# Optimization experiments

Measured on AMD Instinct MI355X. Metric: run time of the kernel, lower is better.

The kernel has to match this reference:

```python
import jax, jax.numpy as jnp
import numpy as np

KERNEL_MUL = 2.0
KERNEL_NUM = 5
THRESH = 0.5            # cfg.FIXED_CONFIDENCE_THRESHOLD
LAMBDA = 1.0            # cfg.ECDA_CLASS_ATTENTION_LAMBDA
GAMMA = 0.1             # cfg.ECDA_COMPACTNESS_WEIGHT_GAMMA
DELTA = 0.01            # cfg.ECDA_REPULSION_WEIGHT_DELTA
NUM_CLASSES = 8
N, D = 2048, 256


def _sqdist(a, b):
    # pairwise squared euclidean distances [Na, Nb]
    d2 = (jnp.sum(a * a, 1)[:, None] + jnp.sum(b * b, 1)[None, :]
          - 2.0 * (a @ b.T))
    return jnp.maximum(d2, 0.0)


def setup_inputs() -> dict:
    key = jax.random.key(0)
    ks = jax.random.split(key, 6)
    return {
        'clean_feats': jax.random.normal(ks[0], (N, D), dtype=jnp.float32),
        'noisy_feats': jax.random.normal(ks[1], (N, D), dtype=jnp.float32),
        'clean_labels': jax.random.randint(ks[2], (N,), 0, NUM_CLASSES),
        'noisy_labels': jax.random.randint(ks[3], (N,), 0, NUM_CLASSES),
        'noisy_mask': jax.random.uniform(ks[4], (N,), dtype=jnp.float32),
        'noisy_scores': jax.random.uniform(ks[5], (N,), dtype=jnp.float32),
        'class_weights_wce': jax.random.uniform(jax.random.fold_in(key, 7), (NUM_CLASSES,), dtype=jnp.float32),
    }


def reference(clean_feats, noisy_feats, clean_labels, noisy_labels,
              noisy_mask, noisy_scores, class_weights_wce):
    C = class_weights_wce.shape[0]
    mask_n = noisy_mask > THRESH                       # float mask -> bool (cfg threshold)

    # full pairwise squared-distance matrices, reused by every class
    D_cc = _sqdist(clean_feats, clean_feats)           # [Nc, Nc]
    D_nn = _sqdist(noisy_feats, noisy_feats)           # [Nn, Nn]
    D_cn = _sqdist(clean_feats, noisy_feats)           # [Nc, Nn]

    classes = jnp.arange(C)
    Ms = (clean_labels[None, :] == classes[:, None]).astype(jnp.float32)   # [C, Nc]
    Mn = ((noisy_labels[None, :] == classes[:, None]) & mask_n[None, :]).astype(jnp.float32)  # [C, Nn]

    # noisy centroids + repulsion over valid classes (torch.pdist mean, negated)
    counts_n = Mn.sum(1)
    centroids = (Mn @ noisy_feats) / jnp.maximum(counts_n, 1.0)[:, None]
    valid = counts_n > 0
    Dcen = jnp.sqrt(jnp.maximum(_sqdist(centroids, centroids), 1e-12))
    pair = jnp.triu(jnp.ones((C, C), bool), 1) & valid[:, None] & valid[None, :]
    npairs = pair.sum().astype(jnp.float32)
    repulsion = jnp.where(valid.sum() > 1,
                          -jnp.sum(jnp.where(pair, Dcen, 0.0)) / jnp.maximum(npairs, 1.0),
                          0.0)

    attn = jnp.exp(LAMBDA * (class_weights_wce.mean() - class_weights_wce))
    half = KERNEL_MUL ** (KERNEL_NUM // 2)

    total = jnp.float32(0.0)
    for c in range(C):
        ms = Ms[c]                                     # clean weights (ones, masked)
        mn = Mn[c]
        n_s, n_t = ms.sum(), mn.sum()
        n = n_s + n_t
        # bandwidth from subset L2 sum (detached, as in .data)
        sumL2 = ms @ (D_cc @ ms) + mn @ (D_nn @ mn) + 2.0 * (ms @ (D_cn @ mn))
        sumL2 = jax.lax.stop_gradient(sumL2)
        bw0 = sumL2 / jnp.maximum(n * n - n, 1.0) / half
        wn = noisy_scores * mn                          # masked noisy weights
        ss = tt = st = jnp.float32(0.0)
        for k in range(KERNEL_NUM):
            bw = bw0 * (KERNEL_MUL ** k) + 1e-8
            ss = ss + ms @ (jnp.exp(-D_cc / bw) @ ms)
            tt = tt + wn @ (jnp.exp(-D_nn / bw) @ wn)
            st = st + ms @ (jnp.exp(-D_cn / bw) @ wn)
        sw = wn.sum()
        term_ss = ss / (n_s * n_s + 1e-8)
        term_tt = tt / (sw * sw + 1e-8)
        term_st = st / (n_s * sw + 1e-8)
        mmd = term_ss + term_tt - 2.0 * term_st
        compact = jnp.sum(mn * jnp.sum((noisy_feats - centroids[c]) ** 2, 1)) / jnp.maximum(n_t, 1.0)
        loss_c = mmd + GAMMA * compact + DELTA * repulsion
        total = total + jnp.where((n_s >= 2) & (n_t >= 2), attn[c] * loss_c, 0.0)
    return total
```

## Files before the change

kernel.cpp:

```cpp
#include <hip/hip_runtime.h>
#include <math.h>


static constexpr int NC = 8;
static constexpr int NN = 2048;
static constexpr int DD = 256;

static constexpr int OFF_CNT_S = 0;
static constexpr int OFF_CNT_T = 64;
static constexpr int OFF_SW    = 128;
static constexpr int OFF_COEF  = 192;
static constexpr int OFF_CCOMP = 256;
static constexpr int OFF_SQSP  = 1024;
static constexpr int OFF_SQTP  = 1536;
static constexpr int OFF_HDR   = 2048;
static constexpr int OFF_VSP   = 4096;
static constexpr int OFF_VTP   = 135168;
static constexpr int OFF_VS    = 266240;
static constexpr int OFF_VT    = 274432;
static constexpr int OFF_QBFS  = 282624;
static constexpr int OFF_QBFT  = 348160;
static constexpr int OFF_WTP   = 413696;
static constexpr size_t OFF_PKS = 479232;
static constexpr size_t OFF_PKT = 8867840;

typedef __attribute__((ext_vector_type(8))) short bf16x8;
typedef __attribute__((ext_vector_type(4))) float f32x4;

__device__ inline float wred64(float v) {
  for (int o = 32; o > 0; o >>= 1) v += __shfl_xor(v, o, 64);
  return v;
}
__device__ inline float brs256(float v, float* sh4) {
  for (int o = 32; o > 0; o >>= 1) v += __shfl_xor(v, o, 64);
  int w = threadIdx.x >> 6, ln = threadIdx.x & 63;
  __syncthreads();
  if (ln == 0) sh4[w] = v;
  __syncthreads();
  float r = 0.f;
  if (threadIdx.x == 0) r = sh4[0] + sh4[1] + sh4[2] + sh4[3];
  return r;
}

__global__ __launch_bounds__(256) void ecda_pack(
    const float* __restrict__ cfeat, const float* __restrict__ nfeat,
    const int* __restrict__ clab, const int* __restrict__ nlab,
    const float* __restrict__ nmask, const float* __restrict__ nscore,
    char* __restrict__ ws, float* __restrict__ out) {
  __shared__ int   ls_idx[NN];
  __shared__ float ls_wt[NN];
  __shared__ int   ls_cntw[4];
  __shared__ float ls_mom[4][256];
  __shared__ float ls_sq[4];
  __shared__ float sh4[4];
  int tid = threadIdx.x, bx = blockIdx.x;
  int wv = tid >> 6, lane = tid & 63;
  int typ = bx >> 7, c = (bx >> 4) & 7, chunk = bx & 15;

  if (bx == 0 && tid == 0) out[0] = 0.f;

  const int* labs = typ ? nlab : clab;
  const float* feats = typ ? nfeat : cfeat;

  int rb = wv * 512;
  int lv[8]; float mv[8], sv[8];
#pragma unroll
  for (int it = 0; it < 8; ++it) {
    int i = rb + it * 64 + lane;
    lv[it] = labs[i];
    if (typ) { mv[it] = nmask[i]; sv[it] = nscore[i]; }
  }
  unsigned long long msks[8];
  int cntw = 0;
#pragma unroll
  for (int it = 0; it < 8; ++it) {
    bool m = (lv[it] == c) && (!typ || mv[it] > 0.5f);
    msks[it] = __ballot(m);
    cntw += __popcll(msks[it]);
  }
  if (lane == 0) ls_cntw[wv] = cntw;
  __syncthreads();
  int base = 0;
  for (int w2 = 0; w2 < wv; ++w2) base += ls_cntw[w2];
#pragma unroll
  for (int it = 0; it < 8; ++it) {
    bool m = (msks[it] >> lane) & 1ull;
    int pos = __popcll(msks[it] & ((1ull << lane) - 1ull));
    if (m) {
      ls_idx[base + pos] = rb + it * 64 + lane;
      ls_wt[base + pos] = typ ? sv[it] : 1.f;
    }
    base += __popcll(msks[it]);
  }
  __syncthreads();
  int count = ls_cntw[0] + ls_cntw[1] + ls_cntw[2] + ls_cntw[3];

  if (chunk == 0) {
    if (tid == 0) (typ ? (int*)(ws + OFF_CNT_T) : (int*)(ws + OFF_CNT_S))[c] = count;
    if (typ) {
      float s = 0.f;
      for (int i = tid; i < count; i += 256) s += ls_wt[i];
      s = brs256(s, sh4);
      if (tid == 0) ((float*)(ws + OFF_SW))[c] = s;
    }
  }

  unsigned short* pk = (unsigned short*)(ws + (typ ? OFF_PKT : OFF_PKS)) + (size_t)c * NN * DD;
  float* qarr = (float*)(ws + (typ ? OFF_QBFT : OFF_QBFS)) + c * NN;
  float* wtp  = (float*)(ws + OFF_WTP) + c * NN;
  float vax = 0.f, vay = 0.f, vaz = 0.f, vaw = 0.f, sqa = 0.f;
  int mstart = chunk * 4 + wv;
  for (int m0 = mstart; m0 < count; m0 += 256) {
    int mm[4]; bool act[4]; float4 v[4];
#pragma unroll
    for (int b = 0; b < 4; ++b) {
      int m = m0 + b * 64;
      act[b] = (m < count);
      mm[b] = act[b] ? m : m0;
    }
#pragma unroll
    for (int b = 0; b < 4; ++b) {
      int idx = ls_idx[mm[b]];
      v[b] = *(const float4*)&feats[(size_t)idx * DD + lane * 4];
    }
#pragma unroll
    for (int b = 0; b < 4; ++b) {
      float raw = wred64(v[b].x * v[b].x + v[b].y * v[b].y
                       + v[b].z * v[b].z + v[b].w * v[b].w);
      unsigned ux = __float_as_uint(v[b].x); ux = (ux + 0x7fffu + ((ux >> 16) & 1u)) & 0xffff0000u;
      unsigned uy = __float_as_uint(v[b].y); uy = (uy + 0x7fffu + ((uy >> 16) & 1u)) & 0xffff0000u;
      unsigned uz = __float_as_uint(v[b].z); uz = (uz + 0x7fffu + ((uz >> 16) & 1u)) & 0xffff0000u;
      unsigned uw = __float_as_uint(v[b].w); uw = (uw + 0x7fffu + ((uw >> 16) & 1u)) & 0xffff0000u;
      float rx = __uint_as_float(ux), ry = __uint_as_float(uy);
      float rz = __uint_as_float(uz), rw = __uint_as_float(uw);
      float rq = wred64(rx * rx + ry * ry + rz * rz + rw * rw);
      if (act[b]) {
        vax += v[b].x; vay += v[b].y; vaz += v[b].z; vaw += v[b].w;
        sqa += raw;
        ushort4 b4;
        b4.x = (unsigned short)(ux >> 16); b4.y = (unsigned short)(uy >> 16);
        b4.z = (unsigned short)(uz >> 16); b4.w = (unsigned short)(uw >> 16);
        *(ushort4*)&pk[(size_t)mm[b] * DD + lane * 4] = b4;
        if (lane == 0) {
          qarr[mm[b]] = rq;
          if (typ) wtp[mm[b]] = ls_wt[mm[b]];
        }
      }
    }
  }
  ls_mom[wv][lane * 4 + 0] = vax; ls_mom[wv][lane * 4 + 1] = vay;
  ls_mom[wv][lane * 4 + 2] = vaz; ls_mom[wv][lane * 4 + 3] = vaw;
  if (lane == 0) ls_sq[wv] = sqa;
  __syncthreads();
  float s = ls_mom[0][tid] + ls_mom[1][tid] + ls_mom[2][tid] + ls_mom[3][tid];
  float* vp = (float*)(ws + (typ ? OFF_VTP : OFF_VSP)) + (c * 16 + chunk) * 256;
  vp[tid] = s;
  if (tid == 0)
    ((float*)(ws + (typ ? OFF_SQTP : OFF_SQSP)))[c * 16 + chunk] =
        ls_sq[0] + ls_sq[1] + ls_sq[2] + ls_sq[3];
}

__global__ __launch_bounds__(256) void ecda_scalars(
    const float* __restrict__ cw, char* __restrict__ ws) {
  __shared__ float sh4[4];
  int c = blockIdx.x, tid = threadIdx.x;
  const float* vsp = (const float*)(ws + OFF_VSP);
  const float* vtp = (const float*)(ws + OFF_VTP);
  float vsd = 0.f, vtd = 0.f;
#pragma unroll
  for (int ch = 0; ch < 16; ++ch) {
    vsd += vsp[(c * 16 + ch) * 256 + tid];
    vtd += vtp[(c * 16 + ch) * 256 + tid];
  }
  ((float*)(ws + OFF_VS))[c * 256 + tid] = vsd;
  ((float*)(ws + OFF_VT))[c * 256 + tid] = vtd;
  float dss = brs256(vsd * vsd, sh4);
  float dtt = brs256(vtd * vtd, sh4);
  float dst = brs256(vsd * vtd, sh4);
  if (tid == 0) {
    const float* sqsp = (const float*)(ws + OFF_SQSP);
    const float* sqtp = (const float*)(ws + OFF_SQTP);
    float sqs = 0.f, sqt = 0.f;
    for (int ch = 0; ch < 16; ++ch) { sqs += sqsp[c * 16 + ch]; sqt += sqtp[c * 16 + ch]; }
    int nsi = ((const int*)(ws + OFF_CNT_S))[c];
    int nti = ((const int*)(ws + OFF_CNT_T))[c];
    float ns = (float)nsi, nt = (float)nti, n = ns + nt;
    float sumL2 = 2.f * ns * sqs - 2.f * dss
                + 2.f * nt * sqt - 2.f * dtt
                + 2.f * (nt * sqs + ns * sqt - 2.f * dst);
    float bw0 = sumL2 / fmaxf(n * n - n, 1.f) * 0.25f;
    float ib[5];
    float mul = 1.f;
    for (int k = 0; k < 5; ++k) { ib[k] = 1.f / (bw0 * mul + 1e-8f); mul *= 2.f; }
    float meanw = 0.f;
    for (int c2 = 0; c2 < NC; ++c2) meanw += cw[c2];
    meanw *= (1.f / NC);
    float attn = expf(meanw - cw[c]);
    float coef = (nsi >= 2 && nti >= 2) ? attn : 0.f;
    float swc = ((const float*)(ws + OFF_SW))[c];
    float scc = coef / (ns * ns + 1e-8f);
    float snn = coef / (swc * swc + 1e-8f);
    float scn = -2.f * coef / (ns * swc + 1e-8f);
    float* hdr = (float*)(ws + OFF_HDR);
    for (int ty = 0; ty < 3; ++ty) {
      float* h = hdr + (ty * 8 + c) * 8;
      int na = (ty == 1) ? nti : nsi;
      int nb = (ty == 0) ? nsi : nti;
      h[0] = __int_as_float(na);
      h[1] = __int_as_float(nb);
      h[2] = (ty == 0) ? scc : (ty == 1) ? snn : scn;
      h[3] = ib[0]; h[4] = ib[1]; h[5] = ib[2]; h[6] = ib[3]; h[7] = ib[4];
    }
    float mx = fmaxf(nt, 1.f);
    float compact = (sqt - 2.f * dtt / mx + nt * dtt / (mx * mx)) / mx;
    ((float*)(ws + OFF_COEF))[c] = coef;
    ((float*)(ws + OFF_CCOMP))[c] = coef * 0.1f * compact;
  }
}

__global__ __launch_bounds__(256) void ecda_pairs(
    char* __restrict__ ws, float* __restrict__ out) {
  __shared__ float shred[4];
  __shared__ float dcen[28];
  int tid = threadIdx.x, bx = blockIdx.x;
  int wv = tid >> 6, lane = tid & 63;

  if (bx == 1536) {
    const int* cnt_t = (const int*)(ws + OFF_CNT_T);
    const float* vt = (const float*)(ws + OFF_VT);
    for (int t = wv; t < 28; t += 4) {
      int a = 0, r = t;
      while (r >= 7 - a) { r -= 7 - a; ++a; }
      int b = a + 1 + r;
      float ima = 1.f / fmaxf((float)cnt_t[a], 1.f);
      float imb = 1.f / fmaxf((float)cnt_t[b], 1.f);
      float4 x = *(const float4*)&vt[a * DD + lane * 4];
      float4 y = *(const float4*)&vt[b * DD + lane * 4];
      float dx = x.x * ima - y.x * imb, dy = x.y * ima - y.y * imb;
      float dz = x.z * ima - y.z * imb, dw = x.w * ima - y.w * imb;
      float s = wred64(dx * dx + dy * dy + dz * dz + dw * dw);
      if (lane == 0) dcen[t] = sqrtf(fmaxf(s, 1e-12f));
    }
    __syncthreads();
    if (tid == 0) {
      int nvalid = 0;
      for (int c = 0; c < NC; ++c) nvalid += (cnt_t[c] > 0);
      float sumD = 0.f; int np = 0; int p = 0;
      for (int a = 0; a < NC; ++a)
        for (int b = a + 1; b < NC; ++b) {
          if (cnt_t[a] > 0 && cnt_t[b] > 0) { sumD += dcen[p]; ++np; }
          ++p;
        }
      float repl = (nvalid > 1) ? (-sumD / fmaxf((float)np, 1.f)) : 0.f;
      const float* coefA = (const float*)(ws + OFF_COEF);
      const float* ccomp = (const float*)(ws + OFF_CCOMP);
      float base = 0.f, csum = 0.f;
      for (int c = 0; c < NC; ++c) { base += ccomp[c]; csum += coefA[c]; }
      base += 0.01f * repl * csum;
      atomicAdd(out, base);
    }
    return;
  }

  int type  = bx >> 9;
  int c     = (bx >> 6) & 7;
  int rtile = (bx >> 3) & 7;
  int ctile = bx & 7;
  if (type <= 1 && ctile < rtile) return;

  const f32x4* H = (const f32x4*)((const char*)ws + OFF_HDR) + (type * 8 + c) * 2;
  f32x4 h0 = H[0];
  int na = __float_as_int(h0[0]);
  int nb = __float_as_int(h0[1]);
  float scale = h0[2];
  int rbase = rtile * 32, cbase = ctile * 32;
  if (scale == 0.f || rbase >= na || cbase >= nb) return;
  f32x4 h1 = H[1];
  float ib0 = h0[3], ib1 = h1[0], ib2 = h1[1], ib3 = h1[2], ib4 = h1[3];
  float factor = (type <= 1 && ctile > rtile) ? 2.f : 1.f;

  const unsigned short* pkS = (const unsigned short*)(ws + OFF_PKS) + (size_t)c * NN * DD;
  const unsigned short* pkT = (const unsigned short*)(ws + OFF_PKT) + (size_t)c * NN * DD;
  const float* qbS = (const float*)(ws + OFF_QBFS) + c * NN;
  const float* qbT = (const float*)(ws + OFF_QBFT) + c * NN;
  const float* wtp = (const float*)(ws + OFF_WTP) + c * NN;
  const unsigned short* pkA = (type == 1) ? pkT : pkS;
  const unsigned short* pkB = (type == 0) ? pkS : pkT;
  const float* qaB = (type == 1) ? qbT : qbS;
  const float* qbB = (type == 0) ? qbS : qbT;

  int sr = (wv >> 1) * 16, sc2 = (wv & 1) * 16;
  int posA = rbase + sr + (lane & 15);
  int posB = cbase + sc2 + (lane & 15);
  int pAc = posA < na ? posA : (na - 1);
  int pBc = posB < nb ? posB : (nb - 1);
  const unsigned short* rowA = pkA + (size_t)pAc * DD + (lane >> 4) * 8;
  const unsigned short* rowB = pkB + (size_t)pBc * DD + (lane >> 4) * 8;

  f32x4 acc = {0.f, 0.f, 0.f, 0.f};
#pragma unroll
  for (int ks = 0; ks < 8; ++ks) {
    bf16x8 af = *(const bf16x8*)(rowA + ks * 32);
    bf16x8 bf = *(const bf16x8*)(rowB + ks * 32);
    acc = __builtin_amdgcn_mfma_f32_16x16x32_bf16(af, bf, acc, 0, 0, 0);
  }

  bool jval = (posB < nb);
  float knj = qbB[pBc];
  float wj = (type == 0) ? 1.f : wtp[pBc];
  int rowbase = rbase + sr + ((lane >> 4) << 2);
  f32x4 qA4 = *(const f32x4*)&qaB[rowbase];
  f32x4 wA4 = {1.f, 1.f, 1.f, 1.f};
  if (type == 1) wA4 = *(const f32x4*)&wtp[rowbase];
  float partial = 0.f;
#pragma unroll
  for (int r = 0; r < 4; ++r) {
    int ip = rowbase + r;
    bool val = jval && (ip < na);
    float d2 = fmaxf(qA4[r] + knj - 2.f * acc[r], 0.f);
    float e = __expf(-d2 * ib0) + __expf(-d2 * ib1) + __expf(-d2 * ib2)
            + __expf(-d2 * ib3) + __expf(-d2 * ib4);
    float wgt = (type == 1) ? wA4[r] * wj : wj;
    partial += val ? wgt * e : 0.f;
  }
  partial = wred64(partial);
  if (lane == 0) shred[wv] = partial;
  __syncthreads();
  if (tid == 0) {
    float tot = shred[0] + shred[1] + shred[2] + shred[3];
    atomicAdd(out, scale * factor * tot);
  }
}

extern "C" void kernel_launch(void* const* d_in, const int* in_sizes, int n_in,
                              void* d_out, int out_size, void* d_ws, size_t ws_size,
                              hipStream_t stream) {
  const float* cfeat  = (const float*)d_in[0];
  const float* nfeat  = (const float*)d_in[1];
  const int*   clab   = (const int*)d_in[2];
  const int*   nlab   = (const int*)d_in[3];
  const float* nmask  = (const float*)d_in[4];
  const float* nscore = (const float*)d_in[5];
  const float* cw     = (const float*)d_in[6];
  float* out = (float*)d_out;
  char* ws = (char*)d_ws;

  ecda_pack<<<256, 256, 0, stream>>>(cfeat, nfeat, clab, nlab, nmask, nscore,
                                     ws, out);
  ecda_scalars<<<8, 256, 0, stream>>>(cw, ws);
  ecda_pairs<<<1537, 256, 0, stream>>>(ws, out);
}
```

Measured before the change: 34.07 us.

## Fold per-class scalar and repulsion stage into pack kernel via last-block ticket

Removes the separate 8-block scalars kernel by having the last block of the pack kernel (chosen with an atomic ticket counter) compute the per-class bandwidths, headers, compactness and the centroid repulsion term. The repulsion block is also removed from the pairwise kernel, which now launches one fewer block. This saves a kernel launch and its dependency gap, in exchange for a serial tail in one block. The ticket counter is never reset, so correctness relies on the modulo-256 check holding across repeated calls, and it assumes the workspace starts zeroed.

```diff
diff --git a/kernel.cpp b/kernel.cpp
--- a/kernel.cpp
+++ b/kernel.cpp
@@ -9,14 +9,12 @@
 static constexpr int OFF_CNT_S = 0;
 static constexpr int OFF_CNT_T = 64;
 static constexpr int OFF_SW    = 128;
-static constexpr int OFF_COEF  = 192;
-static constexpr int OFF_CCOMP = 256;
 static constexpr int OFF_SQSP  = 1024;
 static constexpr int OFF_SQTP  = 1536;
 static constexpr int OFF_HDR   = 2048;
+static constexpr int OFF_TICKET= 3072;
 static constexpr int OFF_VSP   = 4096;
 static constexpr int OFF_VTP   = 135168;
-static constexpr int OFF_VS    = 266240;
 static constexpr int OFF_VT    = 274432;
 static constexpr int OFF_QBFS  = 282624;
 static constexpr int OFF_QBFT  = 348160;
@@ -46,13 +44,15 @@
     const float* __restrict__ cfeat, const float* __restrict__ nfeat,
     const int* __restrict__ clab, const int* __restrict__ nlab,
     const float* __restrict__ nmask, const float* __restrict__ nscore,
-    char* __restrict__ ws, float* __restrict__ out) {
+    const float* __restrict__ cw, char* __restrict__ ws,
+    float* __restrict__ out) {
   __shared__ int   ls_idx[NN];
   __shared__ float ls_wt[NN];
   __shared__ int   ls_cntw[4];
   __shared__ float ls_mom[4][256];
   __shared__ float ls_sq[4];
   __shared__ float sh4[4];
+  __shared__ float dcen[28];
   int tid = threadIdx.x, bx = blockIdx.x;
   int wv = tid >> 6, lane = tid & 63;
   int typ = bx >> 7, c = (bx >> 4) & 7, chunk = bx & 15;
@@ -158,109 +158,112 @@
   if (tid == 0)
     ((float*)(ws + (typ ? OFF_SQTP : OFF_SQSP)))[c * 16 + chunk] =
         ls_sq[0] + ls_sq[1] + ls_sq[2] + ls_sq[3];
-}
-
-__global__ __launch_bounds__(256) void ecda_scalars(
-    const float* __restrict__ cw, char* __restrict__ ws) {
-  __shared__ float sh4[4];
-  int c = blockIdx.x, tid = threadIdx.x;
+
+  __syncthreads();
+  __shared__ unsigned s_tkt;
+  __threadfence();
+  if (tid == 0) s_tkt = atomicAdd((unsigned*)(ws + OFF_TICKET), 1u);
+  __syncthreads();
+  if ((s_tkt & 255u) != 255u) return;
+  __threadfence();
+
   const float* vsp = (const float*)(ws + OFF_VSP);
   const float* vtp = (const float*)(ws + OFF_VTP);
-  float vsd = 0.f, vtd = 0.f;
-#pragma unroll
-  for (int ch = 0; ch < 16; ++ch) {
-    vsd += vsp[(c * 16 + ch) * 256 + tid];
-    vtd += vtp[(c * 16 + ch) * 256 + tid];
-  }
-  ((float*)(ws + OFF_VS))[c * 256 + tid] = vsd;
-  ((float*)(ws + OFF_VT))[c * 256 + tid] = vtd;
-  float dss = brs256(vsd * vsd, sh4);
-  float dtt = brs256(vtd * vtd, sh4);
-  float dst = brs256(vsd * vtd, sh4);
+  const float* sqsp = (const float*)(ws + OFF_SQSP);
+  const float* sqtp = (const float*)(ws + OFF_SQTP);
+  const int* cnt_s = (const int*)(ws + OFF_CNT_S);
+  const int* cnt_t = (const int*)(ws + OFF_CNT_T);
+  float* vtR = (float*)(ws + OFF_VT);
+  float* hdr = (float*)(ws + OFF_HDR);
+  __shared__ float sh_coef[8], sh_ccomp[8];
+
+  for (int r = 0; r < 2; ++r) {
+    int cc = wv * 2 + r;
+    int d0 = lane * 4;
+    f32x4 vsd = {0.f, 0.f, 0.f, 0.f}, vtd = {0.f, 0.f, 0.f, 0.f};
+#pragma unroll
+    for (int ch = 0; ch < 16; ++ch) {
+      vsd += *(const f32x4*)&vsp[(cc * 16 + ch) * 256 + d0];
+      vtd += *(const f32x4*)&vtp[(cc * 16 + ch) * 256 + d0];
+    }
+    *(f32x4*)&vtR[cc * 256 + d0] = vtd;
+    float dss = wred64(vsd[0]*vsd[0] + vsd[1]*vsd[1] + vsd[2]*vsd[2] + vsd[3]*vsd[3]);
+    float dtt = wred64(vtd[0]*vtd[0] + vtd[1]*vtd[1] + vtd[2]*vtd[2] + vtd[3]*vtd[3]);
+    float dst = wred64(vsd[0]*vtd[0] + vsd[1]*vtd[1] + vsd[2]*vtd[2] + vsd[3]*vtd[3]);
+    float sqs = wred64((lane < 16) ? sqsp[cc * 16 + lane] : 0.f);
+    float sqt = wred64((lane < 16) ? sqtp[cc * 16 + lane] : 0.f);
+    if (lane == 0) {
+      int nsi = cnt_s[cc], nti = cnt_t[cc];
+      float ns = (float)nsi, nt = (float)nti, n = ns + nt;
+      float sumL2 = 2.f * ns * sqs - 2.f * dss
+                  + 2.f * nt * sqt - 2.f * dtt
+                  + 2.f * (nt * sqs + ns * sqt - 2.f * dst);
+      float bw0 = sumL2 / fmaxf(n * n - n, 1.f) * 0.25f;
+      float ib[5];
+      float mul = 1.f;
+      for (int k = 0; k < 5; ++k) { ib[k] = 1.f / (bw0 * mul + 1e-8f); mul *= 2.f; }
+      float meanw = 0.f;
+      for (int c2 = 0; c2 < NC; ++c2) meanw += cw[c2];
+      meanw *= (1.f / NC);
+      float attn = expf(meanw - cw[cc]);
+      float coef = (nsi >= 2 && nti >= 2) ? attn : 0.f;
+      float swc = ((const float*)(ws + OFF_SW))[cc];
+      float scc = coef / (ns * ns + 1e-8f);
+      float snn = coef / (swc * swc + 1e-8f);
+      float scn = -2.f * coef / (ns * swc + 1e-8f);
+      for (int ty = 0; ty < 3; ++ty) {
+        float* h = hdr + (ty * 8 + cc) * 8;
+        int na = (ty == 1) ? nti : nsi;
+        int nb = (ty == 0) ? nsi : nti;
+        h[0] = __int_as_float(na);
+        h[1] = __int_as_float(nb);
+        h[2] = (ty == 0) ? scc : (ty == 1) ? snn : scn;
+        h[3] = ib[0]; h[4] = ib[1]; h[5] = ib[2]; h[6] = ib[3]; h[7] = ib[4];
+      }
+      float mx = fmaxf(nt, 1.f);
+      float compact = (sqt - 2.f * dtt / mx + nt * dtt / (mx * mx)) / mx;
+      sh_coef[cc] = coef;
+      sh_ccomp[cc] = coef * 0.1f * compact;
+    }
+  }
+  __syncthreads();
+
+  for (int t = wv; t < 28; t += 4) {
+    int a = 0, r = t;
+    while (r >= 7 - a) { r -= 7 - a; ++a; }
+    int b = a + 1 + r;
+    float ima = 1.f / fmaxf((float)cnt_t[a], 1.f);
+    float imb = 1.f / fmaxf((float)cnt_t[b], 1.f);
+    float4 x = *(const float4*)&vtR[a * DD + lane * 4];
+    float4 y = *(const float4*)&vtR[b * DD + lane * 4];
+    float dx = x.x * ima - y.x * imb, dy = x.y * ima - y.y * imb;
+    float dz = x.z * ima - y.z * imb, dw = x.w * ima - y.w * imb;
+    float ssum = wred64(dx * dx + dy * dy + dz * dz + dw * dw);
+    if (lane == 0) dcen[t] = sqrtf(fmaxf(ssum, 1e-12f));
+  }
+  __syncthreads();
   if (tid == 0) {
-    const float* sqsp = (const float*)(ws + OFF_SQSP);
-    const float* sqtp = (const float*)(ws + OFF_SQTP);
-    float sqs = 0.f, sqt = 0.f;
-    for (int ch = 0; ch < 16; ++ch) { sqs += sqsp[c * 16 + ch]; sqt += sqtp[c * 16 + ch]; }
-    int nsi = ((const int*)(ws + OFF_CNT_S))[c];
-    int nti = ((const int*)(ws + OFF_CNT_T))[c];
-    float ns = (float)nsi, nt = (float)nti, n = ns + nt;
-    float sumL2 = 2.f * ns * sqs - 2.f * dss
-                + 2.f * nt * sqt - 2.f * dtt
-                + 2.f * (nt * sqs + ns * sqt - 2.f * dst);
-    float bw0 = sumL2 / fmaxf(n * n - n, 1.f) * 0.25f;
-    float ib[5];
-    float mul = 1.f;
-    for (int k = 0; k < 5; ++k) { ib[k] = 1.f / (bw0 * mul + 1e-8f); mul *= 2.f; }
-    float meanw = 0.f;
-    for (int c2 = 0; c2 < NC; ++c2) meanw += cw[c2];
-    meanw *= (1.f / NC);
-    float attn = expf(meanw - cw[c]);
-    float coef = (nsi >= 2 && nti >= 2) ? attn : 0.f;
-    float swc = ((const float*)(ws + OFF_SW))[c];
-    float scc = coef / (ns * ns + 1e-8f);
-    float snn = coef / (swc * swc + 1e-8f);
-    float scn = -2.f * coef / (ns * swc + 1e-8f);
-    float* hdr = (float*)(ws + OFF_HDR);
-    for (int ty = 0; ty < 3; ++ty) {
-      float* h = hdr + (ty * 8 + c) * 8;
-      int na = (ty == 1) ? nti : nsi;
-      int nb = (ty == 0) ? nsi : nti;
-      h[0] = __int_as_float(na);
-      h[1] = __int_as_float(nb);
-      h[2] = (ty == 0) ? scc : (ty == 1) ? snn : scn;
-      h[3] = ib[0]; h[4] = ib[1]; h[5] = ib[2]; h[6] = ib[3]; h[7] = ib[4];
-    }
-    float mx = fmaxf(nt, 1.f);
-    float compact = (sqt - 2.f * dtt / mx + nt * dtt / (mx * mx)) / mx;
-    ((float*)(ws + OFF_COEF))[c] = coef;
-    ((float*)(ws + OFF_CCOMP))[c] = coef * 0.1f * compact;
+    int nvalid = 0;
+    for (int c2 = 0; c2 < NC; ++c2) nvalid += (cnt_t[c2] > 0);
+    float sumD = 0.f; int np = 0; int p = 0;
+    for (int a = 0; a < NC; ++a)
+      for (int b = a + 1; b < NC; ++b) {
+        if (cnt_t[a] > 0 && cnt_t[b] > 0) { sumD += dcen[p]; ++np; }
+        ++p;
+      }
+    float repl = (nvalid > 1) ? (-sumD / fmaxf((float)np, 1.f)) : 0.f;
+    float base2 = 0.f, csum = 0.f;
+    for (int c2 = 0; c2 < NC; ++c2) { base2 += sh_ccomp[c2]; csum += sh_coef[c2]; }
+    base2 += 0.01f * repl * csum;
+    atomicAdd(out, base2);
   }
 }
 
 __global__ __launch_bounds__(256) void ecda_pairs(
     char* __restrict__ ws, float* __restrict__ out) {
   __shared__ float shred[4];
-  __shared__ float dcen[28];
   int tid = threadIdx.x, bx = blockIdx.x;
   int wv = tid >> 6, lane = tid & 63;
-
-  if (bx == 1536) {
-    const int* cnt_t = (const int*)(ws + OFF_CNT_T);
-    const float* vt = (const float*)(ws + OFF_VT);
-    for (int t = wv; t < 28; t += 4) {
-      int a = 0, r = t;
-      while (r >= 7 - a) { r -= 7 - a; ++a; }
-      int b = a + 1 + r;
-      float ima = 1.f / fmaxf((float)cnt_t[a], 1.f);
-      float imb = 1.f / fmaxf((float)cnt_t[b], 1.f);
-      float4 x = *(const float4*)&vt[a * DD + lane * 4];
-      float4 y = *(const float4*)&vt[b * DD + lane * 4];
-      float dx = x.x * ima - y.x * imb, dy = x.y * ima - y.y * imb;
-      float dz = x.z * ima - y.z * imb, dw = x.w * ima - y.w * imb;
-      float s = wred64(dx * dx + dy * dy + dz * dz + dw * dw);
-      if (lane == 0) dcen[t] = sqrtf(fmaxf(s, 1e-12f));
-    }
-    __syncthreads();
-    if (tid == 0) {
-      int nvalid = 0;
-      for (int c = 0; c < NC; ++c) nvalid += (cnt_t[c] > 0);
-      float sumD = 0.f; int np = 0; int p = 0;
-      for (int a = 0; a < NC; ++a)
-        for (int b = a + 1; b < NC; ++b) {
-          if (cnt_t[a] > 0 && cnt_t[b] > 0) { sumD += dcen[p]; ++np; }
-          ++p;
-        }
-      float repl = (nvalid > 1) ? (-sumD / fmaxf((float)np, 1.f)) : 0.f;
-      const float* coefA = (const float*)(ws + OFF_COEF);
-      const float* ccomp = (const float*)(ws + OFF_CCOMP);
-      float base = 0.f, csum = 0.f;
-      for (int c = 0; c < NC; ++c) { base += ccomp[c]; csum += coefA[c]; }
-      base += 0.01f * repl * csum;
-      atomicAdd(out, base);
-    }
-    return;
-  }
 
   int type  = bx >> 9;
   int c     = (bx >> 6) & 7;
@@ -346,7 +349,6 @@
   char* ws = (char*)d_ws;
 
   ecda_pack<<<256, 256, 0, stream>>>(cfeat, nfeat, clab, nlab, nmask, nscore,
-                                     ws, out);
-  ecda_scalars<<<8, 256, 0, stream>>>(cw, ws);
-  ecda_pairs<<<1537, 256, 0, stream>>>(ws, out);
-}
+                                     cw, ws, out);
+  ecda_pairs<<<1536, 256, 0, stream>>>(ws, out);
+}
```

After: 57.46 us. 1.69x slower.

## Loop column tiles per block in pair kernel, reusing A fragments in registers

Applied to the files above, without the earlier changes.

The pair kernel now launches 385 blocks instead of 1537. Each block keeps its row-tile A fragments in registers and walks half of the column tiles (split by parity), accumulating locally. This cuts block launch and early-exit overhead, avoids reloading A, and reduces atomics, and blocks with a zero total now skip the atomic entirely. In the pack kernel, the per-row wave reduction for the squared norm is replaced by a per-lane accumulation followed by one reduction. The cost is longer serial work per block, fewer blocks for latency hiding, and some load imbalance across triangular tiles.

```diff
diff --git a/kernel.cpp b/kernel.cpp
--- a/kernel.cpp
+++ b/kernel.cpp
@@ -108,7 +108,7 @@
   unsigned short* pk = (unsigned short*)(ws + (typ ? OFF_PKT : OFF_PKS)) + (size_t)c * NN * DD;
   float* qarr = (float*)(ws + (typ ? OFF_QBFT : OFF_QBFS)) + c * NN;
   float* wtp  = (float*)(ws + OFF_WTP) + c * NN;
-  float vax = 0.f, vay = 0.f, vaz = 0.f, vaw = 0.f, sqa = 0.f;
+  float vax = 0.f, vay = 0.f, vaz = 0.f, vaw = 0.f, qlane = 0.f;
   int mstart = chunk * 4 + wv;
   for (int m0 = mstart; m0 < count; m0 += 256) {
     int mm[4]; bool act[4]; float4 v[4];
@@ -125,8 +125,6 @@
     }
 #pragma unroll
     for (int b = 0; b < 4; ++b) {
-      float raw = wred64(v[b].x * v[b].x + v[b].y * v[b].y
-                       + v[b].z * v[b].z + v[b].w * v[b].w);
       unsigned ux = __float_as_uint(v[b].x); ux = (ux + 0x7fffu + ((ux >> 16) & 1u)) & 0xffff0000u;
       unsigned uy = __float_as_uint(v[b].y); uy = (uy + 0x7fffu + ((uy >> 16) & 1u)) & 0xffff0000u;
       unsigned uz = __float_as_uint(v[b].z); uz = (uz + 0x7fffu + ((uz >> 16) & 1u)) & 0xffff0000u;
@@ -136,7 +134,7 @@
       float rq = wred64(rx * rx + ry * ry + rz * rz + rw * rw);
       if (act[b]) {
         vax += v[b].x; vay += v[b].y; vaz += v[b].z; vaw += v[b].w;
-        sqa += raw;
+        qlane += v[b].x * v[b].x + v[b].y * v[b].y + v[b].z * v[b].z + v[b].w * v[b].w;
         ushort4 b4;
         b4.x = (unsigned short)(ux >> 16); b4.y = (unsigned short)(uy >> 16);
         b4.z = (unsigned short)(uz >> 16); b4.w = (unsigned short)(uw >> 16);
@@ -148,6 +146,7 @@
       }
     }
   }
+  float sqa = wred64(qlane);
   ls_mom[wv][lane * 4 + 0] = vax; ls_mom[wv][lane * 4 + 1] = vay;
   ls_mom[wv][lane * 4 + 2] = vaz; ls_mom[wv][lane * 4 + 3] = vaw;
   if (lane == 0) ls_sq[wv] = sqa;
@@ -219,13 +218,14 @@
 }
 
 __global__ __launch_bounds__(256) void ecda_pairs(
-    char* __restrict__ ws, float* __restrict__ out) {
+    const float* __restrict__ cw, char* __restrict__ ws,
+    float* __restrict__ out) {
   __shared__ float shred[4];
   __shared__ float dcen[28];
   int tid = threadIdx.x, bx = blockIdx.x;
   int wv = tid >> 6, lane = tid & 63;
 
-  if (bx == 1536) {
+  if (bx == 384) {
     const int* cnt_t = (const int*)(ws + OFF_CNT_T);
     const float* vt = (const float*)(ws + OFF_VT);
     for (int t = wv; t < 28; t += 4) {
@@ -238,13 +238,13 @@
       float4 y = *(const float4*)&vt[b * DD + lane * 4];
       float dx = x.x * ima - y.x * imb, dy = x.y * ima - y.y * imb;
       float dz = x.z * ima - y.z * imb, dw = x.w * ima - y.w * imb;
-      float s = wred64(dx * dx + dy * dy + dz * dz + dw * dw);
-      if (lane == 0) dcen[t] = sqrtf(fmaxf(s, 1e-12f));
+      float ssum = wred64(dx * dx + dy * dy + dz * dz + dw * dw);
+      if (lane == 0) dcen[t] = sqrtf(fmaxf(ssum, 1e-12f));
     }
     __syncthreads();
     if (tid == 0) {
       int nvalid = 0;
-      for (int c = 0; c < NC; ++c) nvalid += (cnt_t[c] > 0);
+      for (int c2 = 0; c2 < NC; ++c2) nvalid += (cnt_t[c2] > 0);
       float sumD = 0.f; int np = 0; int p = 0;
       for (int a = 0; a < NC; ++a)
         for (int b = a + 1; b < NC; ++b) {
@@ -254,30 +254,31 @@
       float repl = (nvalid > 1) ? (-sumD / fmaxf((float)np, 1.f)) : 0.f;
       const float* coefA = (const float*)(ws + OFF_COEF);
       const float* ccomp = (const float*)(ws + OFF_CCOMP);
-      float base = 0.f, csum = 0.f;
-      for (int c = 0; c < NC; ++c) { base += ccomp[c]; csum += coefA[c]; }
-      base += 0.01f * repl * csum;
-      atomicAdd(out, base);
+      float base2 = 0.f, csum = 0.f;
+      for (int c2 = 0; c2 < NC; ++c2) { base2 += ccomp[c2]; csum += coefA[c2]; }
+      base2 += 0.01f * repl * csum;
+      atomicAdd(out, base2);
     }
     return;
   }
 
-  int type  = bx >> 9;
-  int c     = (bx >> 6) & 7;
-  int rtile = (bx >> 3) & 7;
-  int ctile = bx & 7;
-  if (type <= 1 && ctile < rtile) return;
+  int par   = bx & 1;
+  int rtile = (bx >> 1) & 7;
+  int c     = (bx >> 4) & 7;
+  int type  = bx >> 7;
 
   const f32x4* H = (const f32x4*)((const char*)ws + OFF_HDR) + (type * 8 + c) * 2;
   f32x4 h0 = H[0];
   int na = __float_as_int(h0[0]);
   int nb = __float_as_int(h0[1]);
   float scale = h0[2];
-  int rbase = rtile * 32, cbase = ctile * 32;
-  if (scale == 0.f || rbase >= na || cbase >= nb) return;
+  int rbase = rtile * 32;
+  if (scale == 0.f || rbase >= na || nb <= 0) return;
+  int ct0 = (type <= 1) ? rtile : 0;
+  int nbt = (nb + 31) >> 5;
+  if (ct0 + par >= nbt) return;
   f32x4 h1 = H[1];
   float ib0 = h0[3], ib1 = h1[0], ib2 = h1[1], ib3 = h1[2], ib4 = h1[3];
-  float factor = (type <= 1 && ctile > rtile) ? 2.f : 1.f;
 
   const unsigned short* pkS = (const unsigned short*)(ws + OFF_PKS) + (size_t)c * NN * DD;
   const unsigned short* pkT = (const unsigned short*)(ws + OFF_PKT) + (size_t)c * NN * DD;
@@ -291,44 +292,51 @@
 
   int sr = (wv >> 1) * 16, sc2 = (wv & 1) * 16;
   int posA = rbase + sr + (lane & 15);
-  int posB = cbase + sc2 + (lane & 15);
   int pAc = posA < na ? posA : (na - 1);
-  int pBc = posB < nb ? posB : (nb - 1);
   const unsigned short* rowA = pkA + (size_t)pAc * DD + (lane >> 4) * 8;
-  const unsigned short* rowB = pkB + (size_t)pBc * DD + (lane >> 4) * 8;
-
-  f32x4 acc = {0.f, 0.f, 0.f, 0.f};
-#pragma unroll
-  for (int ks = 0; ks < 8; ++ks) {
-    bf16x8 af = *(const bf16x8*)(rowA + ks * 32);
-    bf16x8 bf = *(const bf16x8*)(rowB + ks * 32);
-    acc = __builtin_amdgcn_mfma_f32_16x16x32_bf16(af, bf, acc, 0, 0, 0);
-  }
-
-  bool jval = (posB < nb);
-  float knj = qbB[pBc];
-  float wj = (type == 0) ? 1.f : wtp[pBc];
+  bf16x8 afr[8];
+#pragma unroll
+  for (int ks = 0; ks < 8; ++ks) afr[ks] = *(const bf16x8*)(rowA + ks * 32);
   int rowbase = rbase + sr + ((lane >> 4) << 2);
   f32x4 qA4 = *(const f32x4*)&qaB[rowbase];
   f32x4 wA4 = {1.f, 1.f, 1.f, 1.f};
   if (type == 1) wA4 = *(const f32x4*)&wtp[rowbase];
-  float partial = 0.f;
-#pragma unroll
-  for (int r = 0; r < 4; ++r) {
-    int ip = rowbase + r;
-    bool val = jval && (ip < na);
-    float d2 = fmaxf(qA4[r] + knj - 2.f * acc[r], 0.f);
-    float e = __expf(-d2 * ib0) + __expf(-d2 * ib1) + __expf(-d2 * ib2)
-            + __expf(-d2 * ib3) + __expf(-d2 * ib4);
-    float wgt = (type == 1) ? wA4[r] * wj : wj;
-    partial += val ? wgt * e : 0.f;
-  }
-  partial = wred64(partial);
-  if (lane == 0) shred[wv] = partial;
+
+  float lacc = 0.f;
+  for (int ctile = ct0 + par; ctile < nbt; ctile += 2) {
+    int cbase = ctile * 32;
+    int posB = cbase + sc2 + (lane & 15);
+    int pBc = posB < nb ? posB : (nb - 1);
+    const unsigned short* rowB = pkB + (size_t)pBc * DD + (lane >> 4) * 8;
+    f32x4 acc = {0.f, 0.f, 0.f, 0.f};
+#pragma unroll
+    for (int ks = 0; ks < 8; ++ks) {
+      bf16x8 bf = *(const bf16x8*)(rowB + ks * 32);
+      acc = __builtin_amdgcn_mfma_f32_16x16x32_bf16(afr[ks], bf, acc, 0, 0, 0);
+    }
+    bool jval = (posB < nb);
+    float knj = qbB[pBc];
+    float wj = (type == 0) ? 1.f : wtp[pBc];
+    float factor = (type <= 1 && ctile > rtile) ? 2.f : 1.f;
+    float partial = 0.f;
+#pragma unroll
+    for (int r = 0; r < 4; ++r) {
+      int ip = rowbase + r;
+      bool val = jval && (ip < na);
+      float d2 = fmaxf(qA4[r] + knj - 2.f * acc[r], 0.f);
+      float e = __expf(-d2 * ib0) + __expf(-d2 * ib1) + __expf(-d2 * ib2)
+              + __expf(-d2 * ib3) + __expf(-d2 * ib4);
+      float wgt = (type == 1) ? wA4[r] * wj : wj;
+      partial += val ? wgt * e : 0.f;
+    }
+    lacc += factor * partial;
+  }
+  lacc = wred64(lacc);
+  if (lane == 0) shred[wv] = lacc;
   __syncthreads();
   if (tid == 0) {
     float tot = shred[0] + shred[1] + shred[2] + shred[3];
-    atomicAdd(out, scale * factor * tot);
+    if (tot != 0.f) atomicAdd(out, scale * tot);
   }
 }
 
@@ -348,5 +356,5 @@
   ecda_pack<<<256, 256, 0, stream>>>(cfeat, nfeat, clab, nlab, nmask, nscore,
                                      ws, out);
   ecda_scalars<<<8, 256, 0, stream>>>(cw, ws);
-  ecda_pairs<<<1537, 256, 0, stream>>>(ws, out);
-}
+  ecda_pairs<<<385, 256, 0, stream>>>(cw, ws, out);
+}
```

Result: faster. 27.71 us (median of 2 runs) (-18.7%).
